# Performance work log

Measured on AMD Instinct MI355X. Metric: run time of the kernel, lower is better.

The kernel has to match this reference:

```python
import jax, jax.numpy as jnp
import numpy as np

DEPTH, DIM, HEADS, MLP_HID, POS_DIM, PROJ_DIM, NCLS, INP = 5, 128, 8, 256, 128, 128, 1000, 35
EPS = 1e-5

def _ln(x, g, b):
    m = x.mean(-1, keepdims=True)
    v = ((x - m) ** 2).mean(-1, keepdims=True)
    return (x - m) / jnp.sqrt(v + EPS) * g + b

def _gelu(x):
    return jax.nn.gelu(x, approximate=False)  # torch nn.GELU default (erf)

def setup_inputs() -> dict:
    key = jax.random.key(0)
    ks = iter(jax.random.split(key, 80))
    nxt = lambda: next(ks)
    B, N = 8, 1024
    w = lambda *s: (jax.random.normal(nxt(), s, jnp.float32) / np.sqrt(s[-2]).astype(np.float32))
    z = lambda *s: jnp.zeros(s, jnp.float32)
    o = lambda *s: jnp.ones(s, jnp.float32)
    node_feat = jax.random.normal(nxt(), (B, N, 3), jnp.float32)
    a = (jax.random.uniform(nxt(), (B, N, N)) < 0.01).astype(jnp.float32)
    adj = jnp.maximum(a, a.transpose(0, 2, 1))  # symmetric 0/1 adjacency
    lapl = jax.random.normal(nxt(), (B, N, 32), jnp.float32) * 0.1
    d = dict(
        node_feat=node_feat, adj=adj, lapl=lapl,
        cls_token=jax.random.normal(nxt(), (1, 1, DIM), jnp.float32),
        pe_w1=w(INP, 2 * INP), pe_b1=z(2 * INP),
        pe_w2=w(2 * INP, 2 * INP), pe_b2=z(2 * INP),
        pe_w3=w(2 * INP, 2 * INP), pe_b3=z(2 * INP),
        pe_lng=o(2 * INP), pe_lnb=z(2 * INP),
        pe_w4=w(2 * INP, POS_DIM), pe_b4=z(POS_DIM),
        blk_ln1_g=o(DEPTH, DIM), blk_ln1_b=z(DEPTH, DIM),
        blk_qkv_w=w(DEPTH, DIM, 3 * HEADS * DIM),
        blk_proj_w=w(DEPTH, HEADS * DIM, DIM), blk_proj_b=z(DEPTH, DIM),
        blk_gamma_w=jax.random.uniform(nxt(), (DEPTH, DIM, 2), jnp.float32) * 0.01,
        blk_gamma_b=z(DEPTH, 2),
        blk_ln2_g=o(DEPTH, DIM), blk_ln2_b=z(DEPTH, DIM),
        blk_mlp_w1=w(DEPTH, DIM, MLP_HID), blk_mlp_b1=z(DEPTH, MLP_HID),
        blk_mlp_w2=w(DEPTH, MLP_HID, DIM), blk_mlp_b2=z(DEPTH, DIM),
        head_lng=o(DIM), head_lnb=z(DIM), head_w=w(DIM, DIM), head_b=z(DIM),
        proj_w1=w(DIM, PROJ_DIM), proj_b1=z(PROJ_DIM),
        proj_w2=w(PROJ_DIM, PROJ_DIM), proj_b2=z(PROJ_DIM),
        proj_w3=w(PROJ_DIM, PROJ_DIM), proj_b3=z(PROJ_DIM),
        proj_lng=o(PROJ_DIM), proj_lnb=z(PROJ_DIM),
        proj_w4=w(PROJ_DIM, NCLS), proj_b4=z(NCLS),
    )
    return d

def reference(node_feat, adj, lapl, cls_token, pe_w1, pe_b1, pe_w2, pe_b2, pe_w3, pe_b3,
              pe_lng, pe_lnb, pe_w4, pe_b4, blk_ln1_g, blk_ln1_b, blk_qkv_w, blk_proj_w,
              blk_proj_b, blk_gamma_w, blk_gamma_b, blk_ln2_g, blk_ln2_b, blk_mlp_w1,
              blk_mlp_b1, blk_mlp_w2, blk_mlp_b2, head_lng, head_lnb, head_w, head_b,
              proj_w1, proj_b1, proj_w2, proj_b2, proj_w3, proj_b3, proj_lng, proj_lnb,
              proj_w4, proj_b4):
    B, N, _ = node_feat.shape
    M = N + 1
    # positional-encoding MLP on concatenated [node_feat | lapl] (inp_dim = 35)
    x = jnp.concatenate([node_feat, lapl], axis=2)
    x = _gelu(x @ pe_w1 + pe_b1)
    x = _gelu(x @ pe_w2 + pe_b2)
    x = _gelu(x @ pe_w3 + pe_b3)
    x = _ln(x, pe_lng, pe_lnb) @ pe_w4 + pe_b4  # [B,N,DIM]
    x = jnp.concatenate([jnp.broadcast_to(cls_token, (B, 1, DIM)), x], axis=1)  # [B,M,DIM]
    # adjacency with cls row/col, adj_cls[:,0,0] = 1
    adj_cls = jnp.zeros((B, M, M), x.dtype).at[:, 0, 0].set(1.0).at[:, 1:, 1:].set(adj)
    scale = DIM ** (-0.5)
    for i in range(DEPTH):
        h = _ln(x, blk_ln1_g[i], blk_ln1_b[i])
        qkv = (h @ blk_qkv_w[i]).reshape(B, M, 3, HEADS, DIM).transpose(2, 0, 3, 1, 4)
        q, k, v = qkv[0], qkv[1], qkv[2]  # each [B,H,M,D]
        attn = jnp.einsum('bhnd,bhmd->bhnm', q, k) * scale
        gamma = jnp.exp(h @ blk_gamma_w[i] + blk_gamma_b[i])  # [B,M,2], use_exp=True
        attn = gamma[:, None, :, 0:1] * attn + gamma[:, None, :, 1:2] * adj_cls[:, None]
        attn = jax.nn.softmax(attn, axis=-1)
        o = jnp.einsum('bhnm,bhmd->bhnd', attn, v).transpose(0, 2, 1, 3).reshape(B, M, HEADS * DIM)
        x = o @ blk_proj_w[i] + blk_proj_b[i] + h  # residual from normed input (as in source)
        h2 = _ln(x, blk_ln2_g[i], blk_ln2_b[i])
        x = _gelu(h2 @ blk_mlp_w1[i] + blk_mlp_b1[i]) @ blk_mlp_w2[i] + blk_mlp_b2[i] + h2
    c = x[:, 0]
    c = _ln(c, head_lng, head_lnb) @ head_w + head_b  # mlp_head
    p = _gelu(c @ proj_w1 + proj_b1)
    p = _gelu(p @ proj_w2 + proj_b2)
    p = _gelu(p @ proj_w3 + proj_b3)
    p = _ln(p, proj_lng, proj_lnb) @ proj_w4 + proj_b4
    return (c, p)
```

## Files before the change

### kernel.cpp

```cpp
#include <hip/hip_runtime.h>
#include <hip/hip_bf16.h>
#include <math.h>

#define NB 8
#define NSEQ 1024
#define M_ 1025
#define ROWS (NB * M_)
#define DIMC 128
#define NHEADS 8
#define QKV3 3072
#define PEROWS (NB * NSEQ)
#define ACS 1088

typedef __attribute__((ext_vector_type(8))) short bf16x8;
typedef __attribute__((ext_vector_type(4))) float f32x4;

__device__ __forceinline__ float gelu_f(float x) {
  return 0.5f * x * (1.f + erff(x * 0.70710678118654752440f));
}

__device__ __forceinline__ unsigned short f2bf(float f) {
  __hip_bfloat16 h = __float2bfloat16(f);
  return *reinterpret_cast<unsigned short*>(&h);
}

__device__ __forceinline__ float bf2f(unsigned short u) {
  union { unsigned int i; float f; } c;
  c.i = ((unsigned int)u) << 16;
  return c.f;
}

__device__ __forceinline__ void g2lds16(const void* g, void* l) {
  __builtin_amdgcn_global_load_lds(
      (__attribute__((address_space(1))) void*)(g),
      (__attribute__((address_space(3))) void*)(l), 16, 0, 0);
}

__global__ __launch_bounds__(128) void pe_fused_k(
    const float* __restrict__ nf, const float* __restrict__ lp,
    const float* __restrict__ w1, const float* __restrict__ b1,
    const float* __restrict__ w2, const float* __restrict__ b2,
    const float* __restrict__ w3, const float* __restrict__ b3,
    const float* __restrict__ lng, const float* __restrict__ lnb,
    const float* __restrict__ w4, const float* __restrict__ b4,
    float* __restrict__ x)
{
  __shared__ float sA[16][36];
  __shared__ float sB[16][72];
  __shared__ float sC[16][72];
  const int tid = threadIdx.x;
  const int r0 = blockIdx.x * 16;

  for (int i = tid; i < 16 * 35; i += 128) {
    const int r = i / 35, c = i - r * 35;
    const int gr = r0 + r;
    sA[r][c] = (c < 3) ? nf[(size_t)gr * 3 + c] : lp[(size_t)gr * 32 + (c - 3)];
  }
  __syncthreads();
  if (tid < 70) {
    float acc[16];
#pragma unroll
    for (int r = 0; r < 16; ++r) acc[r] = b1[tid];
    for (int k = 0; k < 35; ++k) {
      const float wv = w1[k * 70 + tid];
#pragma unroll
      for (int r = 0; r < 16; ++r) acc[r] = fmaf(sA[r][k], wv, acc[r]);
    }
#pragma unroll
    for (int r = 0; r < 16; ++r) sB[r][tid] = gelu_f(acc[r]);
  }
  __syncthreads();
  if (tid < 70) {
    float acc[16];
#pragma unroll
    for (int r = 0; r < 16; ++r) acc[r] = b2[tid];
    for (int k = 0; k < 70; ++k) {
      const float wv = w2[k * 70 + tid];
#pragma unroll
      for (int r = 0; r < 16; ++r) acc[r] = fmaf(sB[r][k], wv, acc[r]);
    }
#pragma unroll
    for (int r = 0; r < 16; ++r) sC[r][tid] = gelu_f(acc[r]);
  }
  __syncthreads();
  if (tid < 70) {
    float acc[16];
#pragma unroll
    for (int r = 0; r < 16; ++r) acc[r] = b3[tid];
    for (int k = 0; k < 70; ++k) {
      const float wv = w3[k * 70 + tid];
#pragma unroll
      for (int r = 0; r < 16; ++r) acc[r] = fmaf(sC[r][k], wv, acc[r]);
    }
#pragma unroll
    for (int r = 0; r < 16; ++r) sB[r][tid] = gelu_f(acc[r]);
  }
  __syncthreads();
  if (tid < 16) {
    float m = 0.f;
    for (int d = 0; d < 70; ++d) m += sB[tid][d];
    m *= (1.f / 70.f);
    float v = 0.f;
    for (int d = 0; d < 70; ++d) { const float t = sB[tid][d] - m; v += t * t; }
    const float inv = rsqrtf(v * (1.f / 70.f) + 1e-5f);
    for (int d = 0; d < 70; ++d) sB[tid][d] = (sB[tid][d] - m) * inv * lng[d] + lnb[d];
  }
  __syncthreads();
  {
    float acc[16];
#pragma unroll
    for (int r = 0; r < 16; ++r) acc[r] = b4[tid];
    for (int k = 0; k < 70; ++k) {
      const float wv = w4[k * 128 + tid];
#pragma unroll
      for (int r = 0; r < 16; ++r) acc[r] = fmaf(sB[r][k], wv, acc[r]);
    }
#pragma unroll
    for (int r = 0; r < 16; ++r) {
      const int gr = r0 + r;
      x[(size_t)(gr + gr / 1024 + 1) * DIMC + tid] = acc[r];
    }
  }
}

template<int ACT, int OBF, int RES>
__global__ __launch_bounds__(256) void mgemm_k(
    const unsigned short* __restrict__ Xb, const unsigned short* __restrict__ Wt,
    const float* __restrict__ bias, const float* __restrict__ res,
    void* __restrict__ outp, int rows, int K, int N)
{
  __shared__ unsigned short sX[64][72];
  __shared__ unsigned short sW[64][72];
  const int tid = threadIdx.x;
  const int w = tid >> 6, lane = tid & 63;
  const int col = lane & 15, quad = lane >> 4;
  const int r0 = blockIdx.x * 64, n0 = blockIdx.y * 64;
  const int lr = tid >> 2, lc = tid & 3;
  const int xrow = min(r0 + lr, rows - 1);
  const unsigned short* xsrc = Xb + (size_t)xrow * K + lc * 8;
  const unsigned short* wsrc = Wt + (size_t)(n0 + lr) * K + lc * 8;

  f32x4 acc[4];
#pragma unroll
  for (int t = 0; t < 4; ++t) acc[t] = (f32x4){0.f, 0.f, 0.f, 0.f};

  for (int k0 = 0; k0 < K; k0 += 64) {
    __syncthreads();
    *(uint4*)&sX[lr][lc * 8]      = *(const uint4*)(xsrc + k0);
    *(uint4*)&sX[lr][lc * 8 + 32] = *(const uint4*)(xsrc + k0 + 32);
    *(uint4*)&sW[lr][lc * 8]      = *(const uint4*)(wsrc + k0);
    *(uint4*)&sW[lr][lc * 8 + 32] = *(const uint4*)(wsrc + k0 + 32);
    __syncthreads();
    const bf16x8 aX0 = *(const bf16x8*)&sX[w * 16 + col][quad * 8];
    const bf16x8 aX1 = *(const bf16x8*)&sX[w * 16 + col][32 + quad * 8];
#pragma unroll
    for (int t = 0; t < 4; ++t) {
      const bf16x8 bW0 = *(const bf16x8*)&sW[t * 16 + col][quad * 8];
      const bf16x8 bW1 = *(const bf16x8*)&sW[t * 16 + col][32 + quad * 8];
      acc[t] = __builtin_amdgcn_mfma_f32_16x16x32_bf16(aX0, bW0, acc[t], 0, 0, 0);
      acc[t] = __builtin_amdgcn_mfma_f32_16x16x32_bf16(aX1, bW1, acc[t], 0, 0, 0);
    }
  }
  const int gr_base = r0 + w * 16 + quad * 4;
#pragma unroll
  for (int t = 0; t < 4; ++t) {
    const int n = n0 + t * 16 + col;
    const float bv = bias ? bias[n] : 0.f;
#pragma unroll
    for (int r = 0; r < 4; ++r) {
      const int gr = gr_base + r;
      if (gr < rows) {
        float v = acc[t][r] + bv;
        if (ACT) v = gelu_f(v);
        if (RES) v += res[(size_t)gr * N + n];
        if (OBF) ((unsigned short*)outp)[(size_t)gr * N + n] = f2bf(v);
        else     ((float*)outp)[(size_t)gr * N + n] = v;
      }
    }
  }
}

template<int OBF, int VT>
__global__ __launch_bounds__(256) void mgemm128_k(
    const unsigned short* __restrict__ Xb, const unsigned short* __restrict__ Wt,
    const float* __restrict__ bias, void* __restrict__ outp,
    unsigned short* __restrict__ vtp, int rows, int K, int N)
{
  __shared__ unsigned short sX[128][72];
  __shared__ unsigned short sW[128][72];
  const int tid = threadIdx.x;
  const int w = tid >> 6, lane = tid & 63;
  const int col = lane & 15, quad = lane >> 4;
  const int wr = w >> 1, wc = w & 1;
  const int r0 = blockIdx.x * 128, n0 = blockIdx.y * 128;

  f32x4 acc[4][4];
#pragma unroll
  for (int i = 0; i < 4; ++i)
#pragma unroll
    for (int j = 0; j < 4; ++j) acc[i][j] = (f32x4){0.f, 0.f, 0.f, 0.f};

  for (int k0 = 0; k0 < K; k0 += 64) {
    __syncthreads();
#pragma unroll
    for (int l = 0; l < 4; ++l) {
      const int idx = l * 256 + tid;
      const int row = idx >> 3, c = idx & 7;
      const int xrow = min(r0 + row, rows - 1);
      *(uint4*)&sX[row][c * 8] = *(const uint4*)(Xb + (size_t)xrow * K + k0 + c * 8);
      *(uint4*)&sW[row][c * 8] = *(const uint4*)(Wt + (size_t)(n0 + row) * K + k0 + c * 8);
    }
    __syncthreads();
    bf16x8 aX[4][2];
#pragma unroll
    for (int i = 0; i < 4; ++i) {
      aX[i][0] = *(const bf16x8*)&sX[wr * 64 + i * 16 + col][quad * 8];
      aX[i][1] = *(const bf16x8*)&sX[wr * 64 + i * 16 + col][32 + quad * 8];
    }
#pragma unroll
    for (int j = 0; j < 4; ++j) {
      const bf16x8 b0 = *(const bf16x8*)&sW[wc * 64 + j * 16 + col][quad * 8];
      const bf16x8 b1 = *(const bf16x8*)&sW[wc * 64 + j * 16 + col][32 + quad * 8];
#pragma unroll
      for (int i = 0; i < 4; ++i) {
        acc[i][j] = __builtin_amdgcn_mfma_f32_16x16x32_bf16(aX[i][0], b0, acc[i][j], 0, 0, 0);
        acc[i][j] = __builtin_amdgcn_mfma_f32_16x16x32_bf16(aX[i][1], b1, acc[i][j], 0, 0, 0);
      }
    }
  }
  const bool dovt = VT && (n0 >= 2048);
#pragma unroll
  for (int i = 0; i < 4; ++i) {
    const int gr_base = r0 + wr * 64 + i * 16 + quad * 4;
    int bb[4], mm[4];
    if (dovt) {
#pragma unroll
      for (int r = 0; r < 4; ++r) {
        const int gr = gr_base + r;
        bb[r] = gr / 1025;
        mm[r] = gr - bb[r] * 1025;
      }
    }
#pragma unroll
    for (int j = 0; j < 4; ++j) {
      const int n = n0 + wc * 64 + j * 16 + col;
      const float bv = bias ? bias[n] : 0.f;
      const int hh = (n - 2048) >> 7;
      const int d  = (n - 2048) & 127;
#pragma unroll
      for (int r = 0; r < 4; ++r) {
        const int gr = gr_base + r;
        if (gr < rows) {
          const float v = acc[i][j][r] + bv;
          const unsigned short bf = f2bf(v);
          if (OBF) ((unsigned short*)outp)[(size_t)gr * N + n] = bf;
          else     ((float*)outp)[(size_t)gr * N + n] = v;
          if (dovt) vtp[(((size_t)(bb[r] * NHEADS + hh) * DIMC + d) * ACS) + mm[r]] = bf;
        }
      }
    }
  }
}

__global__ __launch_bounds__(256) void ln_rows_k(
    const float* __restrict__ in, float* __restrict__ out,
    unsigned short* __restrict__ outb,
    const float* __restrict__ g, const float* __restrict__ b,
    const float* __restrict__ gw, const float* __restrict__ gb,
    float* __restrict__ gamout, int rows, int D)
{
  const int wv = (blockIdx.x * blockDim.x + threadIdx.x) >> 6;
  const int lane = threadIdx.x & 63;
  if (wv >= rows) return;
  const float* r = in + (size_t)wv * D;
  float s = 0.f;
  for (int d = lane; d < D; d += 64) s += r[d];
  for (int off = 32; off; off >>= 1) s += __shfl_down(s, off);
  const float mean = __shfl(s, 0) / (float)D;
  float v = 0.f;
  for (int d = lane; d < D; d += 64) { float t = r[d] - mean; v += t * t; }
  for (int off = 32; off; off >>= 1) v += __shfl_down(v, off);
  const float inv = rsqrtf(__shfl(v, 0) / (float)D + 1e-5f);
  float* orow = out + (size_t)wv * D;
  float a0 = 0.f, a1 = 0.f;
  for (int d = lane; d < D; d += 64) {
    const float o = (r[d] - mean) * inv * g[d] + b[d];
    orow[d] = o;
    if (outb) outb[(size_t)wv * D + d] = f2bf(o);
    if (gw) { a0 = fmaf(o, gw[2 * d], a0); a1 = fmaf(o, gw[2 * d + 1], a1); }
  }
  if (gw) {
    for (int off = 32; off; off >>= 1) { a0 += __shfl_down(a0, off); a1 += __shfl_down(a1, off); }
    if (lane == 0) {
      gamout[(size_t)wv * 2 + 0] = expf(a0 + gb[0]);
      gamout[(size_t)wv * 2 + 1] = expf(a1 + gb[1]);
    }
  }
}

__global__ __launch_bounds__(256) void adjp_k(const float* __restrict__ adj,
                                              unsigned long long* __restrict__ adjp)
{
  const int n = blockIdx.x;
  const int b = blockIdx.y;
  const int wv = threadIdx.x >> 6, lane = threadIdx.x & 63;
  for (int w = wv; w < 17; w += 4) {
    const int m = w * 64 + lane;
    float av = 0.f;
    if (n == 0) av = (m == 0) ? 1.f : 0.f;
    else if (m >= 1 && m <= NSEQ) av = adj[((size_t)b * NSEQ + (n - 1)) * NSEQ + (m - 1)];
    const unsigned long long mask = __ballot(av != 0.f);
    if (lane == 0) adjp[((size_t)b * M_ + n) * 17 + w] = mask;
  }
}

__global__ void wtrans_k(const float* __restrict__ W, unsigned short* __restrict__ Wt,
                         int K, int N)
{
  __shared__ float t[32][33];
  const int k0 = blockIdx.x * 32, n0 = blockIdx.y * 32;
  const float* Wd = W + (size_t)blockIdx.z * K * N;
  unsigned short* Wtd = Wt + (size_t)blockIdx.z * K * N;
  for (int i = threadIdx.y; i < 32; i += 8)
    t[i][threadIdx.x] = Wd[(size_t)(k0 + i) * N + n0 + threadIdx.x];
  __syncthreads();
  for (int i = threadIdx.y; i < 32; i += 8)
    Wtd[(size_t)(n0 + i) * K + k0 + threadIdx.x] = f2bf(t[threadIdx.x][i]);
}

__global__ __launch_bounds__(512) void attn_mfma_k(
    const unsigned short* __restrict__ qkv, const float* __restrict__ gamma,
    const unsigned long long* __restrict__ adjp, const unsigned short* __restrict__ vt,
    unsigned short* __restrict__ o)
{
  __shared__ unsigned short sK[2][64][128];
  __shared__ unsigned short sVt[128][64];
  __shared__ unsigned short sP[128][64];

  const int hh = blockIdx.x, qt = blockIdx.y, b = blockIdx.z;
  const int tid = threadIdx.x;
  const int w = tid >> 6;
  const int lane = tid & 63;
  const int col = lane & 15;
  const int quad = lane >> 4;
  const int n0 = qt * 128;
  const int qbase = n0 + w * 16;
  const float scale = 0.088388347648318447f;

  bf16x8 aQ[4];
  {
    const int qrow = min(qbase + col, 1024);
    const unsigned short* qp = qkv + ((size_t)(b * M_ + qrow)) * QKV3 + hh * DIMC + quad * 8;
#pragma unroll
    for (int c = 0; c < 4; ++c) aQ[c] = *(const bf16x8*)(qp + c * 32);
  }
  float g0[4], g1[4];
  size_t adjo[4];
#pragma unroll
  for (int r = 0; r < 4; ++r) {
    const int nc = min(qbase + quad * 4 + r, 1024);
    g0[r] = gamma[(size_t)(b * M_ + nc) * 2 + 0] * scale;
    g1[r] = gamma[(size_t)(b * M_ + nc) * 2 + 1];
    adjo[r] = ((size_t)b * M_ + nc) * 17;
  }

  float l_i[4] = {0.f, 0.f, 0.f, 0.f};
  f32x4 Oacc[8];
#pragma unroll
  for (int t = 0; t < 8; ++t) Oacc[t] = (f32x4){0.f, 0.f, 0.f, 0.f};

  const size_t vtbase = ((size_t)(b * NHEADS + hh)) * DIMC * ACS;

  auto stageK = [&](int buf, int kt_) {
#pragma unroll
    for (int l = 0; l < 2; ++l) {
      const int m = l * 32 + w * 4 + (lane >> 4);
      const int gm = min(kt_ * 64 + m, 1024);
      const unsigned short* src = qkv + ((size_t)(b * M_ + gm)) * QKV3 + 1024
                                  + hh * DIMC + (((lane & 15) ^ (m & 7)) * 8);
      g2lds16(src, &sK[buf][l * 32 + w * 4][0]);
    }
  };
  auto stageV = [&](int kt_) {
#pragma unroll
    for (int l = 0; l < 2; ++l) {
      const int d = l * 64 + w * 8 + (lane >> 3);
      const unsigned short* src = vt + vtbase + (size_t)d * ACS + kt_ * 64
                                  + (((lane & 7) ^ (d & 7)) * 8);
      g2lds16(src, &sVt[l * 64 + w * 8][0]);
    }
  };

  stageK(0, 0);
  unsigned long long mk[4];
#pragma unroll
  for (int r = 0; r < 4; ++r) mk[r] = adjp[adjo[r] + 0];

  int cur = 0;
  for (int kt = 0; kt < 17; ++kt) {
    const int m0 = kt * 64;
    __syncthreads();

    stageV(kt);
    const bool more = (kt < 16);
    if (more) stageK(cur ^ 1, kt + 1);

    f32x4 Sacc[4];
#pragma unroll
    for (int t = 0; t < 4; ++t) Sacc[t] = (f32x4){0.f, 0.f, 0.f, 0.f};
    __builtin_amdgcn_s_setprio(1);
#pragma unroll
    for (int t = 0; t < 4; ++t) {
#pragma unroll
      for (int c = 0; c < 4; ++c) {
        const bf16x8 bK = *(const bf16x8*)&sK[cur][t * 16 + col][((c * 4 + quad) ^ (col & 7)) * 8];
        Sacc[t] = __builtin_amdgcn_mfma_f32_16x16x32_bf16(aQ[c], bK, Sacc[t], 0, 0, 0);
      }
    }
    __builtin_amdgcn_s_setprio(0);

#pragma unroll
    for (int t = 0; t < 4; ++t) {
      const int m = m0 + t * 16 + col;
      const bool mv = (m < M_);
      const int chb = t * 2 + (col >> 3);
      const int sh = t * 16 + col;
#pragma unroll
      for (int r = 0; r < 4; ++r) {
        const float bias = ((mk[r] >> sh) & 1ull) ? g1[r] : 0.f;
        const float s = fmaf(g0[r], Sacc[t][r], bias);
        const float pv = mv ? __expf(s) : 0.f;
        l_i[r] += pv;
        const int ql = w * 16 + quad * 4 + r;
        sP[ql][((chb ^ (ql & 7)) * 8) + (col & 7)] = f2bf(pv);
      }
    }

    if (more) asm volatile("s_waitcnt vmcnt(2)" ::: "memory");
    else      asm volatile("s_waitcnt vmcnt(0)" ::: "memory");
    __builtin_amdgcn_s_barrier();
    __builtin_amdgcn_sched_barrier(0);

    if (more) {
#pragma unroll
      for (int r = 0; r < 4; ++r) mk[r] = adjp[adjo[r] + kt + 1];
    }

    __builtin_amdgcn_s_setprio(1);
#pragma unroll
    for (int ch = 0; ch < 2; ++ch) {
      const int pr = w * 16 + col;
      const bf16x8 aP = *(const bf16x8*)&sP[pr][((ch * 4 + quad) ^ (col & 7)) * 8];
#pragma unroll
      for (int t = 0; t < 8; ++t) {
        const bf16x8 bV = *(const bf16x8*)&sVt[t * 16 + col][((ch * 4 + quad) ^ (col & 7)) * 8];
        Oacc[t] = __builtin_amdgcn_mfma_f32_16x16x32_bf16(aP, bV, Oacc[t], 0, 0, 0);
      }
    }
    __builtin_amdgcn_s_setprio(0);
    cur ^= 1;
  }

#pragma unroll
  for (int r = 0; r < 4; ++r) {
    float s = l_i[r];
    s += __shfl_xor(s, 1);
    s += __shfl_xor(s, 2);
    s += __shfl_xor(s, 4);
    s += __shfl_xor(s, 8);
    const int n = qbase + quad * 4 + r;
    if (n < M_) {
      const float invl = 1.f / s;
      unsigned short* orow = o + ((size_t)(b * M_ + n)) * (NHEADS * DIMC) + hh * DIMC + col;
#pragma unroll
      for (int t = 0; t < 8; ++t) orow[t * 16] = f2bf(Oacc[t][r] * invl);
    }
  }
}

__global__ __launch_bounds__(256) void head_fused_k(
    const float* __restrict__ x,
    const float* __restrict__ hlg, const float* __restrict__ hlb,
    const float* __restrict__ hw, const float* __restrict__ hb,
    const float* __restrict__ pw1, const float* __restrict__ pb1,
    const float* __restrict__ pw2, const float* __restrict__ pb2,
    const float* __restrict__ pw3, const float* __restrict__ pb3,
    const float* __restrict__ plg, const float* __restrict__ plb,
    const float* __restrict__ pw4, const float* __restrict__ pb4,
    float* __restrict__ out_c, float* __restrict__ out_p)
{
  __shared__ float sA[8][128];
  __shared__ float sB[8][128];
  const int tid = threadIdx.x;

  for (int i = tid; i < 8 * 128; i += 256) {
    const int bb = i >> 7, d = i & 127;
    sA[bb][d] = x[(size_t)bb * M_ * DIMC + d];
  }
  __syncthreads();
  if (tid < 8) {
    float m = 0.f;
    for (int d = 0; d < 128; ++d) m += sA[tid][d];
    m *= (1.f / 128.f);
    float v = 0.f;
    for (int d = 0; d < 128; ++d) { const float t = sA[tid][d] - m; v += t * t; }
    const float inv = rsqrtf(v * (1.f / 128.f) + 1e-5f);
    for (int d = 0; d < 128; ++d) sA[tid][d] = (sA[tid][d] - m) * inv * hlg[d] + hlb[d];
  }
  __syncthreads();
  {
    const int j = tid & 127, rb = (tid >> 7) * 4;
    float acc[4];
#pragma unroll
    for (int r = 0; r < 4; ++r) acc[r] = hb[j];
    for (int k = 0; k < 128; ++k) {
      const float wv = hw[k * 128 + j];
#pragma unroll
      for (int r = 0; r < 4; ++r) acc[r] = fmaf(sA[rb + r][k], wv, acc[r]);
    }
#pragma unroll
    for (int r = 0; r < 4; ++r) { sB[rb + r][j] = acc[r]; out_c[(rb + r) * 128 + j] = acc[r]; }
  }
  __syncthreads();
  const float* Ws[3] = {pw1, pw2, pw3};
  const float* Bs[3] = {pb1, pb2, pb3};
  for (int s = 0; s < 3; ++s) {
    const float (*src)[128] = (s & 1) ? sA : sB;
    float (*dst)[128] = (s & 1) ? sB : sA;
    const int j = tid & 127, rb = (tid >> 7) * 4;
    float acc[4];
#pragma unroll
    for (int r = 0; r < 4; ++r) acc[r] = Bs[s][j];
    for (int k = 0; k < 128; ++k) {
      const float wv = Ws[s][k * 128 + j];
#pragma unroll
      for (int r = 0; r < 4; ++r) acc[r] = fmaf(src[rb + r][k], wv, acc[r]);
    }
#pragma unroll
    for (int r = 0; r < 4; ++r) dst[rb + r][j] = gelu_f(acc[r]);
    __syncthreads();
  }
  if (tid < 8) {
    float m = 0.f;
    for (int d = 0; d < 128; ++d) m += sA[tid][d];
    m *= (1.f / 128.f);
    float v = 0.f;
    for (int d = 0; d < 128; ++d) { const float t = sA[tid][d] - m; v += t * t; }
    const float inv = rsqrtf(v * (1.f / 128.f) + 1e-5f);
    for (int d = 0; d < 128; ++d) sA[tid][d] = (sA[tid][d] - m) * inv * plg[d] + plb[d];
  }
  __syncthreads();
  for (int j = tid; j < 1000; j += 256) {
    float acc[8];
#pragma unroll
    for (int bb = 0; bb < 8; ++bb) acc[bb] = pb4[j];
    for (int k = 0; k < 128; ++k) {
      const float wv = pw4[(size_t)k * 1000 + j];
#pragma unroll
      for (int bb = 0; bb < 8; ++bb) acc[bb] = fmaf(sA[bb][k], wv, acc[bb]);
    }
#pragma unroll
    for (int bb = 0; bb < 8; ++bb) out_p[bb * 1000 + j] = acc[bb];
  }
}

__global__ void fill_cls_k(const float* __restrict__ cls, float* __restrict__ x)
{
  x[(size_t)blockIdx.x * M_ * DIMC + threadIdx.x] = cls[threadIdx.x];
}

extern "C" void kernel_launch(void* const* d_in, const int* in_sizes, int n_in,
                              void* d_out, int out_size, void* d_ws, size_t ws_size,
                              hipStream_t stream)
{
  (void)in_sizes; (void)n_in; (void)out_size; (void)ws_size;
  const float* node_feat = (const float*)d_in[0];
  const float* adj       = (const float*)d_in[1];
  const float* lapl      = (const float*)d_in[2];
  const float* cls_token = (const float*)d_in[3];
  const float* pe_w1 = (const float*)d_in[4];
  const float* pe_b1 = (const float*)d_in[5];
  const float* pe_w2 = (const float*)d_in[6];
  const float* pe_b2 = (const float*)d_in[7];
  const float* pe_w3 = (const float*)d_in[8];
  const float* pe_b3 = (const float*)d_in[9];
  const float* pe_lng = (const float*)d_in[10];
  const float* pe_lnb = (const float*)d_in[11];
  const float* pe_w4 = (const float*)d_in[12];
  const float* pe_b4 = (const float*)d_in[13];
  const float* blk_ln1_g = (const float*)d_in[14];
  const float* blk_ln1_b = (const float*)d_in[15];
  const float* blk_qkv_w = (const float*)d_in[16];
  const float* blk_proj_w = (const float*)d_in[17];
  const float* blk_proj_b = (const float*)d_in[18];
  const float* blk_gamma_w = (const float*)d_in[19];
  const float* blk_gamma_b = (const float*)d_in[20];
  const float* blk_ln2_g = (const float*)d_in[21];
  const float* blk_ln2_b = (const float*)d_in[22];
  const float* blk_mlp_w1 = (const float*)d_in[23];
  const float* blk_mlp_b1 = (const float*)d_in[24];
  const float* blk_mlp_w2 = (const float*)d_in[25];
  const float* blk_mlp_b2 = (const float*)d_in[26];
  const float* head_lng = (const float*)d_in[27];
  const float* head_lnb = (const float*)d_in[28];
  const float* head_w = (const float*)d_in[29];
  const float* head_b = (const float*)d_in[30];
  const float* proj_w1 = (const float*)d_in[31];
  const float* proj_b1 = (const float*)d_in[32];
  const float* proj_w2 = (const float*)d_in[33];
  const float* proj_b2 = (const float*)d_in[34];
  const float* proj_w3 = (const float*)d_in[35];
  const float* proj_b3 = (const float*)d_in[36];
  const float* proj_lng = (const float*)d_in[37];
  const float* proj_lnb = (const float*)d_in[38];
  const float* proj_w4 = (const float*)d_in[39];
  const float* proj_b4 = (const float*)d_in[40];

  float* ws   = (float*)d_ws;
  float* x    = ws;
  float* h    = x + 1049600;
  float* gam  = h + 1049600;
  float* obuf = gam + 16400;
  unsigned short* obufb = (unsigned short*)obuf;
  unsigned short* hidb  = (unsigned short*)(obuf + 4198400);
  float* sm  = obuf + 5248000;
  unsigned short* hb   = (unsigned short*)(sm + 8192);
  unsigned short* qkv  = hb + 1049600;
  unsigned long long* adjp = (unsigned long long*)(qkv + 25190400);
  unsigned short* vt   = (unsigned short*)(adjp + 139400 + 88);
  unsigned short* qkvWt = vt + 8912896;
  unsigned short* projWt = qkvWt + 5 * 393216;
  unsigned short* mlp1Wt = projWt + 5 * 131072;
  unsigned short* mlp2Wt = mlp1Wt + 5 * 32768;

  float* out_c = (float*)d_out;
  float* out_p = out_c + NB * DIMC;

  adjp_k<<<dim3(M_, NB), 256, 0, stream>>>(adj, adjp);
  wtrans_k<<<dim3(4, 96, 5), dim3(32, 8), 0, stream>>>(blk_qkv_w, qkvWt, 128, 3072);
  wtrans_k<<<dim3(32, 4, 5), dim3(32, 8), 0, stream>>>(blk_proj_w, projWt, 1024, 128);
  wtrans_k<<<dim3(4, 8, 5), dim3(32, 8), 0, stream>>>(blk_mlp_w1, mlp1Wt, 128, 256);
  wtrans_k<<<dim3(8, 4, 5), dim3(32, 8), 0, stream>>>(blk_mlp_w2, mlp2Wt, 256, 128);

  pe_fused_k<<<512, 128, 0, stream>>>(node_feat, lapl, pe_w1, pe_b1, pe_w2, pe_b2,
                                      pe_w3, pe_b3, pe_lng, pe_lnb, pe_w4, pe_b4, x);
  fill_cls_k<<<NB, DIMC, 0, stream>>>(cls_token, x);

  const int lnGrid = (ROWS * 64 + 255) / 256;
  for (int i = 0; i < 5; ++i) {
    const float* ln1g = blk_ln1_g + i * DIMC;
    const float* ln1b = blk_ln1_b + i * DIMC;
    const float* pb   = blk_proj_b + i * DIMC;
    const float* gw   = blk_gamma_w + (size_t)i * DIMC * 2;
    const float* gb   = blk_gamma_b + i * 2;
    const float* ln2g = blk_ln2_g + i * DIMC;
    const float* ln2b = blk_ln2_b + i * DIMC;
    const float* mb1  = blk_mlp_b1 + i * 256;
    const float* mb2  = blk_mlp_b2 + i * DIMC;
    const unsigned short* qw = qkvWt + (size_t)i * 393216;
    const unsigned short* pw = projWt + (size_t)i * 131072;
    const unsigned short* m1w = mlp1Wt + (size_t)i * 32768;
    const unsigned short* m2w = mlp2Wt + (size_t)i * 32768;

    ln_rows_k<<<lnGrid, 256, 0, stream>>>(x, h, hb, ln1g, ln1b, gw, gb, gam, ROWS, DIMC);
    mgemm128_k<1, 1><<<dim3(65, 24), 256, 0, stream>>>(hb, qw, nullptr, qkv, vt, ROWS, 128, 3072);
    attn_mfma_k<<<dim3(NHEADS, 9, NB), 512, 0, stream>>>(qkv, gam, adjp, vt, obufb);
    mgemm_k<0, 0, 1><<<dim3(129, 2), 256, 0, stream>>>(obufb, pw, pb, h, x, ROWS, 1024, 128);
    ln_rows_k<<<lnGrid, 256, 0, stream>>>(x, h, hb, ln2g, ln2b, nullptr, nullptr, nullptr, ROWS, DIMC);
    mgemm_k<1, 1, 0><<<dim3(129, 4), 256, 0, stream>>>(hb, m1w, mb1, nullptr, hidb, ROWS, 128, 256);
    mgemm_k<0, 0, 1><<<dim3(129, 2), 256, 0, stream>>>(hidb, m2w, mb2, h, x, ROWS, 256, 128);
  }

  head_fused_k<<<1, 256, 0, stream>>>(x, head_lng, head_lnb, head_w, head_b,
                                      proj_w1, proj_b1, proj_w2, proj_b2,
                                      proj_w3, proj_b3, proj_lng, proj_lnb,
                                      proj_w4, proj_b4, out_c, out_p);
}
```

Before: 1.452 ms.

## Split lone tail query row into dedicated single-row attention kernel

The attention grid previously used 9 query tiles of 128 to cover 1025 rows, so the ninth tile did a full K/V sweep for a single valid row. This change shrinks the grid to 8 tiles and drops the clamps and bounds checks. A new small kernel computes the last query row per (batch, head) with scalar dot products and a shared-memory probability buffer. The cost is an extra launch, plus a row ordering that places the last row at index 1024 while the cls row sits at index 0. The softmax in the new kernel skips the max subtraction, relying on bounded logits.

```diff
diff --git a/kernel.cpp b/kernel.cpp
--- a/kernel.cpp
+++ b/kernel.cpp
@@ -349,7 +349,7 @@
 
   bf16x8 aQ[4];
   {
-    const int qrow = min(qbase + col, 1024);
+    const int qrow = qbase + col;
     const unsigned short* qp = qkv + ((size_t)(b * M_ + qrow)) * QKV3 + hh * DIMC + quad * 8;
 #pragma unroll
     for (int c = 0; c < 4; ++c) aQ[c] = *(const bf16x8*)(qp + c * 32);
@@ -358,7 +358,7 @@
   size_t adjo[4];
 #pragma unroll
   for (int r = 0; r < 4; ++r) {
-    const int nc = min(qbase + quad * 4 + r, 1024);
+    const int nc = qbase + quad * 4 + r;
     g0[r] = gamma[(size_t)(b * M_ + nc) * 2 + 0] * scale;
     g1[r] = gamma[(size_t)(b * M_ + nc) * 2 + 1];
     adjo[r] = ((size_t)b * M_ + nc) * 17;
@@ -469,12 +469,70 @@
     s += __shfl_xor(s, 4);
     s += __shfl_xor(s, 8);
     const int n = qbase + quad * 4 + r;
-    if (n < M_) {
-      const float invl = 1.f / s;
-      unsigned short* orow = o + ((size_t)(b * M_ + n)) * (NHEADS * DIMC) + hh * DIMC + col;
-#pragma unroll
-      for (int t = 0; t < 8; ++t) orow[t * 16] = f2bf(Oacc[t][r] * invl);
-    }
+    const float invl = 1.f / s;
+    unsigned short* orow = o + ((size_t)(b * M_ + n)) * (NHEADS * DIMC) + hh * DIMC + col;
+#pragma unroll
+    for (int t = 0; t < 8; ++t) orow[t * 16] = f2bf(Oacc[t][r] * invl);
+  }
+}
+
+__global__ __launch_bounds__(256) void cls_attn_k(
+    const unsigned short* __restrict__ qkv, const float* __restrict__ gamma,
+    const unsigned long long* __restrict__ adjp, const unsigned short* __restrict__ vt,
+    unsigned short* __restrict__ o)
+{
+  __shared__ float qf[DIMC];
+  __shared__ float pbuf[1056];
+  __shared__ float lred[4];
+  __shared__ float oshare[DIMC];
+  const int hh = blockIdx.x & 7, b = blockIdx.x >> 3;
+  const int tid = threadIdx.x;
+  const size_t rowbase = (size_t)b * M_ + 1024;
+
+  if (tid < DIMC) qf[tid] = bf2f(qkv[rowbase * QKV3 + hh * DIMC + tid]);
+  __syncthreads();
+  const float g0 = gamma[rowbase * 2 + 0] * 0.088388347648318447f;
+  const float g1 = gamma[rowbase * 2 + 1];
+
+  float lpart = 0.f;
+  for (int m = tid; m < M_; m += 256) {
+    const unsigned short* kp = qkv + ((size_t)(b * M_ + m)) * QKV3 + 1024 + hh * DIMC;
+    float s = 0.f;
+#pragma unroll
+    for (int d0 = 0; d0 < DIMC; d0 += 8) {
+      const bf16x8 kv = *(const bf16x8*)(kp + d0);
+#pragma unroll
+      for (int j = 0; j < 8; ++j)
+        s = fmaf(bf2f((unsigned short)kv[j]), qf[d0 + j], s);
+    }
+    const unsigned long long mkv = adjp[rowbase * 17 + (m >> 6)];
+    const float bias = ((mkv >> (m & 63)) & 1ull) ? g1 : 0.f;
+    const float p = __expf(fmaf(g0, s, bias));
+    pbuf[m] = p;
+    lpart += p;
+  }
+  for (int off = 32; off; off >>= 1) lpart += __shfl_down(lpart, off);
+  if ((tid & 63) == 0) lred[tid >> 6] = lpart;
+  __syncthreads();
+  const float linv = 1.f / (lred[0] + lred[1] + lred[2] + lred[3]);
+
+  const int d = tid & 127, half = tid >> 7;
+  const unsigned short* vrow = vt + ((size_t)(b * NHEADS + hh)) * DIMC * ACS + (size_t)d * ACS;
+  float acc = 0.f;
+  const int mstart = half * 512;
+  const int mend = half ? 1024 : 512;
+  for (int m0 = mstart; m0 < mend; m0 += 8) {
+    const bf16x8 vv = *(const bf16x8*)(vrow + m0);
+#pragma unroll
+    for (int j = 0; j < 8; ++j)
+      acc = fmaf(bf2f((unsigned short)vv[j]), pbuf[m0 + j], acc);
+  }
+  if (half) acc = fmaf(bf2f(vrow[1024]), pbuf[1024], acc);
+  if (half == 0) oshare[d] = acc;
+  __syncthreads();
+  if (half == 1) {
+    const float val = (oshare[d] + acc) * linv;
+    o[rowbase * (NHEADS * DIMC) + hh * DIMC + d] = f2bf(val);
   }
 }
 
@@ -664,7 +722,8 @@
 
     ln_rows_k<<<lnGrid, 256, 0, stream>>>(x, h, hb, ln1g, ln1b, gw, gb, gam, ROWS, DIMC);
     mgemm128_k<1, 1><<<dim3(65, 24), 256, 0, stream>>>(hb, qw, nullptr, qkv, vt, ROWS, 128, 3072);
-    attn_mfma_k<<<dim3(NHEADS, 9, NB), 512, 0, stream>>>(qkv, gam, adjp, vt, obufb);
+    attn_mfma_k<<<dim3(NHEADS, 8, NB), 512, 0, stream>>>(qkv, gam, adjp, vt, obufb);
+    cls_attn_k<<<64, 256, 0, stream>>>(qkv, gam, adjp, vt, obufb);
     mgemm_k<0, 0, 1><<<dim3(129, 2), 256, 0, stream>>>(obufb, pw, pb, h, x, ROWS, 1024, 128);
     ln_rows_k<<<lnGrid, 256, 0, stream>>>(x, h, hb, ln2g, ln2b, nullptr, nullptr, nullptr, ROWS, DIMC);
     mgemm_k<1, 1, 0><<<dim3(129, 4), 256, 0, stream>>>(hb, m1w, mb1, nullptr, hidb, ROWS, 128, 256);
```

Measured after the change: 1.468 ms. Within noise of the previous version (+1.1%).
